# Optimization experiments

Hardware: AMD Instinct MI355X
Metric: run time of the kernel (lower is better)

## Reference

```python
import jax, jax.numpy as jnp
import numpy as np

NUM_HEADS = 32
HEAD_DIM = 128
ROPE_THETA = 10000.0


def _rope_tables(seq_len, head_dim, dtype):
    # inv freqs: 1 / theta^(2k/d), k = 0..d/2-1
    k = jnp.arange(head_dim // 2, dtype=jnp.float32)
    inv_freq = 1.0 / (ROPE_THETA ** (2.0 * k / head_dim))
    m = jnp.arange(seq_len, dtype=jnp.float32)
    freqs = jnp.outer(m, inv_freq)  # [S, D/2]
    return jnp.cos(freqs).astype(dtype), jnp.sin(freqs).astype(dtype)


def _apply_rope(x, cos, sin):
    # x: [B, H, S, D]; pairs are (x[2k], x[2k+1]) viewed as complex
    x0 = x[..., 0::2]
    x1 = x[..., 1::2]
    # broadcast cos/sin [S, D/2] -> [1, 1, S, D/2]
    out0 = x0 * cos - x1 * sin
    out1 = x0 * sin + x1 * cos
    # re-interleave
    return jnp.stack([out0, out1], axis=-1).reshape(x.shape)


def setup_inputs() -> dict:
    key = jax.random.key(0)
    k1, k2, k3 = jax.random.split(key, 3)
    B, S, D = 2, 2048, 4096
    x = jax.random.normal(k1, (B, S, D), dtype=jnp.float32)
    w_qkv = jax.random.normal(k2, (D, 3 * D), dtype=jnp.float32) * (D ** -0.5)
    w_proj = jax.random.normal(k3, (D, D), dtype=jnp.float32) * (D ** -0.5)
    b_proj = jnp.zeros((D,), dtype=jnp.float32)
    return {"x": x, "w_qkv": w_qkv, "w_proj": w_proj, "b_proj": b_proj}


def reference(x, w_qkv, w_proj, b_proj):
    B, S, D = x.shape
    H, Hd = NUM_HEADS, HEAD_DIM

    qkv = x @ w_qkv                                   # [B, S, 3D]
    qkv = qkv.reshape(B, S, 3, H, Hd)
    qkv = jnp.transpose(qkv, (2, 0, 3, 1, 4))          # [3, B, H, S, Hd]
    q, k, v = qkv[0], qkv[1], qkv[2]

    cos, sin = _rope_tables(S, Hd, x.dtype)
    q = _apply_rope(q, cos, sin)
    k = _apply_rope(k, cos, sin)

    scale = 1.0 / np.sqrt(Hd)
    scores = jnp.einsum('bhqd,bhkd->bhqk', q, k) * scale   # [B, H, S, S]
    causal = jnp.tril(jnp.ones((S, S), dtype=bool))
    scores = jnp.where(causal, scores, jnp.finfo(scores.dtype).min)
    attn = jax.nn.softmax(scores, axis=-1)
    out = jnp.einsum('bhqk,bhkd->bhqd', attn, v)            # [B, H, S, Hd]

    ctx = jnp.transpose(out, (0, 2, 1, 3)).reshape(B, S, H * Hd)
    return ctx @ w_proj + b_proj
```

## Files before the change

kernel.cpp:

```cpp
#include <hip/hip_runtime.h>
#include <stdint.h>

typedef unsigned short ushort_t;
typedef __attribute__((ext_vector_type(8))) short s16x8;
typedef __attribute__((ext_vector_type(4))) float f32x4;
typedef __attribute__((ext_vector_type(4))) unsigned short u16x4;

#define DEV __device__ __forceinline__

DEV ushort_t f2bf(float f) {
  union { float f; uint32_t u; } v; v.f = f;
  uint32_t r = (v.u + 0x7FFFu + ((v.u >> 16) & 1u)) >> 16;
  return (ushort_t)r;
}
DEV float bf2f(ushort_t u) {
  union { uint32_t u; float f; } v; v.u = ((uint32_t)u) << 16;
  return v.f;
}

DEV int swz(int row, int chunk) { return chunk ^ (row & 3) ^ ((row >> 2) & 3); }

#define GLD_LDS16(g, l)                                     \
  __builtin_amdgcn_global_load_lds(                         \
      (const __attribute__((address_space(1))) void*)(g),   \
      (__attribute__((address_space(3))) void*)(l), 16, 0, 0)

#define MFMA16(a, b, c) __builtin_amdgcn_mfma_f32_16x16x32_bf16((a), (b), (c), 0, 0, 0)

__global__ __launch_bounds__(256) void k_conv(const float* __restrict__ in,
                                              ushort_t* __restrict__ out, int n4) {
  int i = blockIdx.x * 256 + threadIdx.x;
  if (i >= n4) return;
  float4 v = ((const float4*)in)[i];
  u16x4 o;
  o[0] = f2bf(v.x); o[1] = f2bf(v.y); o[2] = f2bf(v.z); o[3] = f2bf(v.w);
  *((u16x4*)out + i) = o;
}

__global__ __launch_bounds__(256) void k_transpose_conv(const float* __restrict__ in,
                                                        ushort_t* __restrict__ out,
                                                        int R, int C) {
  __shared__ float tile[64][65];
  int c0 = blockIdx.x * 64, r0 = blockIdx.y * 64;
  int t = threadIdx.x;
#pragma unroll
  for (int i = 0; i < 4; ++i) {
    int e = (i * 256 + t) * 4;
    int rr = e >> 6, cc = e & 63;
    float4 v = *(const float4*)(in + (size_t)(r0 + rr) * C + (c0 + cc));
    tile[rr][cc] = v.x; tile[rr][cc + 1] = v.y;
    tile[rr][cc + 2] = v.z; tile[rr][cc + 3] = v.w;
  }
  __syncthreads();
#pragma unroll
  for (int i = 0; i < 4; ++i) {
    int e = (i * 256 + t) * 4;
    int cc = e >> 6, rr = e & 63;
    u16x4 o;
    o[0] = f2bf(tile[rr][cc]);     o[1] = f2bf(tile[rr + 1][cc]);
    o[2] = f2bf(tile[rr + 2][cc]); o[3] = f2bf(tile[rr + 3][cc]);
    *(u16x4*)(out + (size_t)(c0 + cc) * R + (r0 + rr)) = o;
  }
}

template <bool BF16OUT>
__global__ __launch_bounds__(256, 3) void k_gemm_bt(const ushort_t* __restrict__ A,
                                                    const ushort_t* __restrict__ Bt,
                                                    ushort_t* __restrict__ Cb,
                                                    float* __restrict__ Cf,
                                                    const float* __restrict__ bias,
                                                    int M, int N, int K) {
  __shared__ ushort_t lA[128 * 32];
  __shared__ ushort_t lB[128 * 32];
  int t = threadIdx.x;
  int wv = t >> 6, lane = t & 63, quad = lane >> 4, lrow = lane & 15;
  int wr = wv >> 1, wc = wv & 1;
  int n0 = blockIdx.x * 128, m0 = blockIdx.y * 128;

  f32x4 acc[4][4];
#pragma unroll
  for (int i = 0; i < 4; ++i)
#pragma unroll
    for (int j = 0; j < 4; ++j) acc[i][j] = (f32x4){0.f, 0.f, 0.f, 0.f};

  for (int k0 = 0; k0 < K; k0 += 32) {
    __syncthreads();
#pragma unroll
    for (int c = 0; c < 2; ++c) {
      int se = (c * 256 + t) * 8;
      int row = se >> 5;
      int scn = (se >> 3) & 3;
      int col = swz(row, scn) * 8;
      GLD_LDS16(A + (size_t)(m0 + row) * K + k0 + col, lA + (c * 256 + wv * 64) * 8);
      GLD_LDS16(Bt + (size_t)(n0 + row) * K + k0 + col, lB + (c * 256 + wv * 64) * 8);
    }
    __syncthreads();
    s16x8 af[4], bfr[4];
#pragma unroll
    for (int i = 0; i < 4; ++i) {
      int row = wr * 64 + i * 16 + lrow;
      af[i] = *(const s16x8*)(lA + row * 32 + swz(row, quad) * 8);
    }
#pragma unroll
    for (int j = 0; j < 4; ++j) {
      int row = wc * 64 + j * 16 + lrow;
      bfr[j] = *(const s16x8*)(lB + row * 32 + swz(row, quad) * 8);
    }
#pragma unroll
    for (int i = 0; i < 4; ++i)
#pragma unroll
      for (int j = 0; j < 4; ++j) acc[i][j] = MFMA16(af[i], bfr[j], acc[i][j]);
  }

#pragma unroll
  for (int i = 0; i < 4; ++i)
#pragma unroll
    for (int j = 0; j < 4; ++j)
#pragma unroll
      for (int r = 0; r < 4; ++r) {
        int gr = m0 + wr * 64 + i * 16 + quad * 4 + r;
        int gc = n0 + wc * 64 + j * 16 + lrow;
        if (BF16OUT)
          Cb[(size_t)gr * N + gc] = f2bf(acc[i][j][r]);
        else
          Cf[(size_t)gr * N + gc] = acc[i][j][r] + bias[gc];
      }
}

__global__ __launch_bounds__(256) void k_rope(ushort_t* __restrict__ qkv) {
  int tid = blockIdx.x * 256 + threadIdx.x;
  int p = tid & 63;
  int h = (tid >> 6) & 31;
  int s = (tid >> 11) & 2047;
  int b = tid >> 22;
  size_t base = (size_t)(b * 2048 + s) * 12288 + h * 128 + 2 * p;
  float inv_freq = __expf(-(float)p * 0.14391156509165667f);
  float ang = (float)s * inv_freq;
  float c = cosf(ang), sn = sinf(ang);
  float q0 = bf2f(qkv[base]), q1 = bf2f(qkv[base + 1]);
  qkv[base]        = f2bf(q0 * c - q1 * sn);
  qkv[base + 1]    = f2bf(q0 * sn + q1 * c);
  float k0 = bf2f(qkv[base + 4096]), k1 = bf2f(qkv[base + 4097]);
  qkv[base + 4096] = f2bf(k0 * c - k1 * sn);
  qkv[base + 4097] = f2bf(k0 * sn + k1 * c);
}

__global__ __launch_bounds__(256) void k_build_vt(const ushort_t* __restrict__ qkv,
                                                  ushort_t* __restrict__ vt) {
  const int S = 2048;
  int s0 = blockIdx.x * 64;
  int bh = blockIdx.y;
  int b = bh >> 5, h = bh & 31;
  __shared__ ushort_t tl[64][136];
  int t = threadIdx.x;
  const ushort_t* src = qkv + (size_t)(b * S + s0) * 12288 + 8192 + h * 128;
#pragma unroll
  for (int i = 0; i < 4; ++i) {
    int e = (i * 256 + t) * 8;
    int row = e >> 7, col = e & 127;
    *(s16x8*)&tl[row][col] = *(const s16x8*)(src + (size_t)row * 12288 + col);
  }
  __syncthreads();
  ushort_t* dst = vt + (size_t)bh * 128 * S;
#pragma unroll
  for (int i = 0; i < 4; ++i) {
    int e = (i * 256 + t) * 8;
    int d = e >> 6, ss = e & 63;
    s16x8 o;
#pragma unroll
    for (int j = 0; j < 8; ++j) o[j] = (short)tl[ss + j][d];
    *(s16x8*)(dst + (size_t)d * S + s0 + ss) = o;
  }
}

__global__ __launch_bounds__(256, 2) void k_attn(const ushort_t* __restrict__ qkv,
                                                 const ushort_t* __restrict__ vt,
                                                 ushort_t* __restrict__ ctx) {
  const int S = 2048;
  int qt = blockIdx.x, bh = blockIdx.y;
  int b = bh >> 5, h = bh & 31;
  int q0 = qt * 64;
  int t = threadIdx.x;
  int wv = t >> 6, lane = t & 63, quad = lane >> 4, lrow = lane & 15;

  __shared__ ushort_t lQ[64][136];
  __shared__ ushort_t lK[64][136];
  __shared__ ushort_t lV[128][72];
  __shared__ ushort_t lP[4][16][72];

  const ushort_t* qp = qkv + (size_t)(b * S) * 12288 + h * 128;
  const ushort_t* kp = qp + 4096;
  const ushort_t* vp = vt + (size_t)bh * 128 * S;

#pragma unroll
  for (int i = 0; i < 4; ++i) {
    int e = (i * 256 + t) * 8;
    int row = e >> 7, col = e & 127;
    *(s16x8*)&lQ[row][col] = *(const s16x8*)(qp + (size_t)(q0 + row) * 12288 + col);
  }

  f32x4 O[8];
#pragma unroll
  for (int i = 0; i < 8; ++i) O[i] = (f32x4){0.f, 0.f, 0.f, 0.f};
  float m_i[4], l_i[4];
#pragma unroll
  for (int r = 0; r < 4; ++r) { m_i[r] = -__builtin_inff(); l_i[r] = 0.f; }

  const float scale = 0.08838834764831845f;

  for (int kvt = 0; kvt <= qt; ++kvt) {
    int kv0 = kvt * 64;
    __syncthreads();
#pragma unroll
    for (int i = 0; i < 4; ++i) {
      int e = (i * 256 + t) * 8;
      int row = e >> 7, col = e & 127;
      *(s16x8*)&lK[row][col] = *(const s16x8*)(kp + (size_t)(kv0 + row) * 12288 + col);
    }
#pragma unroll
    for (int i = 0; i < 4; ++i) {
      int e = (i * 256 + t) * 8;
      int d = e >> 6, c = e & 63;
      *(s16x8*)&lV[d][c] = *(const s16x8*)(vp + (size_t)d * S + kv0 + c);
    }
    __syncthreads();

    f32x4 sc[4];
#pragma unroll
    for (int nt = 0; nt < 4; ++nt) sc[nt] = (f32x4){0.f, 0.f, 0.f, 0.f};
#pragma unroll
    for (int ks = 0; ks < 4; ++ks) {
      s16x8 a = *(const s16x8*)&lQ[wv * 16 + lrow][ks * 32 + quad * 8];
#pragma unroll
      for (int nt = 0; nt < 4; ++nt) {
        s16x8 bb = *(const s16x8*)&lK[nt * 16 + lrow][ks * 32 + quad * 8];
        sc[nt] = MFMA16(a, bb, sc[nt]);
      }
    }

    int qr = q0 + wv * 16 + quad * 4;
    float mt[4];
#pragma unroll
    for (int r = 0; r < 4; ++r) mt[r] = -__builtin_inff();
    float pvl[4][4];
#pragma unroll
    for (int nt = 0; nt < 4; ++nt) {
      int kc = kv0 + nt * 16 + lrow;
#pragma unroll
      for (int r = 0; r < 4; ++r) {
        float sv = sc[nt][r] * scale;
        if (kc > qr + r) sv = -__builtin_inff();
        pvl[nt][r] = sv;
        mt[r] = fmaxf(mt[r], sv);
      }
    }
#pragma unroll
    for (int r = 0; r < 4; ++r)
#pragma unroll
      for (int off = 1; off < 16; off <<= 1)
        mt[r] = fmaxf(mt[r], __shfl_xor(mt[r], off, 16));

    float al[4], ls[4];
#pragma unroll
    for (int r = 0; r < 4; ++r) {
      float mn = fmaxf(m_i[r], mt[r]);
      al[r] = __expf(m_i[r] - mn);
      m_i[r] = mn;
      ls[r] = 0.f;
    }
#pragma unroll
    for (int nt = 0; nt < 4; ++nt)
#pragma unroll
      for (int r = 0; r < 4; ++r) {
        float p = __expf(pvl[nt][r] - m_i[r]);
        ushort_t pu = f2bf(p);
        lP[wv][quad * 4 + r][nt * 16 + lrow] = pu;
        ls[r] += bf2f(pu);
      }
#pragma unroll
    for (int r = 0; r < 4; ++r) {
#pragma unroll
      for (int off = 1; off < 16; off <<= 1) ls[r] += __shfl_xor(ls[r], off, 16);
      l_i[r] = al[r] * l_i[r] + ls[r];
    }
#pragma unroll
    for (int f = 0; f < 8; ++f)
#pragma unroll
      for (int r = 0; r < 4; ++r) O[f][r] *= al[r];
    __syncthreads();

#pragma unroll
    for (int ks = 0; ks < 2; ++ks) {
      s16x8 a = *(const s16x8*)&lP[wv][lrow][ks * 32 + quad * 8];
#pragma unroll
      for (int f = 0; f < 8; ++f) {
        s16x8 bb = *(const s16x8*)&lV[f * 16 + lrow][ks * 32 + quad * 8];
        O[f] = MFMA16(a, bb, O[f]);
      }
    }
  }

#pragma unroll
  for (int r = 0; r < 4; ++r) l_i[r] = 1.f / l_i[r];
#pragma unroll
  for (int f = 0; f < 8; ++f)
#pragma unroll
    for (int r = 0; r < 4; ++r) {
      size_t idx = (size_t)(b * S + q0 + wv * 16 + quad * 4 + r) * 4096 + h * 128 + f * 16 + lrow;
      ctx[idx] = f2bf(O[f][r] * l_i[r]);
    }
}

extern "C" void kernel_launch(void* const* d_in, const int* in_sizes, int n_in,
                              void* d_out, int out_size, void* d_ws, size_t ws_size,
                              hipStream_t stream) {
  const float* x      = (const float*)d_in[0];
  const float* w_qkv  = (const float*)d_in[1];
  const float* w_proj = (const float*)d_in[2];
  const float* b_proj = (const float*)d_in[3];
  float* out = (float*)d_out;

  char* ws = (char*)d_ws;
  ushort_t* xb     = (ushort_t*)(ws);
  ushort_t* wqkvt  = (ushort_t*)(ws + 33554432ULL);
  ushort_t* wprojt = (ushort_t*)(ws + 134217728ULL);
  ushort_t* qkvb   = (ushort_t*)(ws + 167772160ULL);
  ushort_t* vt     = (ushort_t*)(ws + 268435456ULL);
  ushort_t* ctx    = (ushort_t*)(ws + 301989888ULL);

  k_conv<<<16384, 256, 0, stream>>>(x, xb, 16777216 / 4);
  k_transpose_conv<<<dim3(192, 64), 256, 0, stream>>>(w_qkv, wqkvt, 4096, 12288);
  k_transpose_conv<<<dim3(64, 64), 256, 0, stream>>>(w_proj, wprojt, 4096, 4096);
  k_gemm_bt<true><<<dim3(96, 32), 256, 0, stream>>>(xb, wqkvt, qkvb, nullptr, nullptr,
                                                    4096, 12288, 4096);
  k_rope<<<32768, 256, 0, stream>>>(qkvb);
  k_build_vt<<<dim3(32, 64), 256, 0, stream>>>(qkvb, vt);
  k_attn<<<dim3(32, 64), 256, 0, stream>>>(qkvb, vt, ctx);
  k_gemm_bt<false><<<dim3(32, 32), 256, 0, stream>>>(ctx, wprojt, nullptr, out, b_proj,
                                                     4096, 4096, 4096);
}
```

Before: 1.424 ms.

## Fuse RoPE into QKV GEMM epilogue and widen attention query tile

Applies RoPE inside the QKV GEMM epilogue, pairing adjacent columns with a lane shuffle, and removes the separate rope kernel together with its read-modify-write pass over Q and K. The attention kernel now handles 128 query rows per block, keeps Q fragments in registers instead of LDS, and loads K and V tiles with direct global-to-LDS loads into XOR-swizzled layouts. This halves the number of K/V tile loads per query and cuts LDS bank conflicts. In exchange it costs more registers (two sets of O accumulators), adds a sincos per output element in the GEMM epilogue, and causal imbalance grows with the coarser query tiles.

```diff
diff --git a/kernel.cpp b/kernel.cpp
--- a/kernel.cpp
+++ b/kernel.cpp
@@ -63,7 +63,7 @@
   }
 }
 
-template <bool BF16OUT>
+template <bool BF16OUT, bool ROPE>
 __global__ __launch_bounds__(256, 3) void k_gemm_bt(const ushort_t* __restrict__ A,
                                                     const ushort_t* __restrict__ Bt,
                                                     ushort_t* __restrict__ Cb,
@@ -112,37 +112,34 @@
       for (int j = 0; j < 4; ++j) acc[i][j] = MFMA16(af[i], bfr[j], acc[i][j]);
   }
 
-#pragma unroll
-  for (int i = 0; i < 4; ++i)
-#pragma unroll
-    for (int j = 0; j < 4; ++j)
+  bool do_rope = ROPE && (n0 < 8192);
+  float sgn_sel = (lrow & 1) ? 1.f : -1.f;
+#pragma unroll
+  for (int j = 0; j < 4; ++j) {
+    int gc = n0 + wc * 64 + j * 16 + lrow;
+    float freq = 0.f;
+    if (do_rope) {
+      int p = (gc & 127) >> 1;
+      freq = __expf(-(float)p * 0.14391156509165667f);
+    }
+#pragma unroll
+    for (int i = 0; i < 4; ++i)
 #pragma unroll
       for (int r = 0; r < 4; ++r) {
         int gr = m0 + wr * 64 + i * 16 + quad * 4 + r;
-        int gc = n0 + wc * 64 + j * 16 + lrow;
+        float val = acc[i][j][r];
+        if (do_rope) {
+          float other = __shfl_xor(val, 1);
+          float sv, cv;
+          sincosf((float)(gr & 2047) * freq, &sv, &cv);
+          val = fmaf(other, sgn_sel * sv, val * cv);
+        }
         if (BF16OUT)
-          Cb[(size_t)gr * N + gc] = f2bf(acc[i][j][r]);
+          Cb[(size_t)gr * N + gc] = f2bf(val);
         else
-          Cf[(size_t)gr * N + gc] = acc[i][j][r] + bias[gc];
-      }
-}
-
-__global__ __launch_bounds__(256) void k_rope(ushort_t* __restrict__ qkv) {
-  int tid = blockIdx.x * 256 + threadIdx.x;
-  int p = tid & 63;
-  int h = (tid >> 6) & 31;
-  int s = (tid >> 11) & 2047;
-  int b = tid >> 22;
-  size_t base = (size_t)(b * 2048 + s) * 12288 + h * 128 + 2 * p;
-  float inv_freq = __expf(-(float)p * 0.14391156509165667f);
-  float ang = (float)s * inv_freq;
-  float c = cosf(ang), sn = sinf(ang);
-  float q0 = bf2f(qkv[base]), q1 = bf2f(qkv[base + 1]);
-  qkv[base]        = f2bf(q0 * c - q1 * sn);
-  qkv[base + 1]    = f2bf(q0 * sn + q1 * c);
-  float k0 = bf2f(qkv[base + 4096]), k1 = bf2f(qkv[base + 4097]);
-  qkv[base + 4096] = f2bf(k0 * c - k1 * sn);
-  qkv[base + 4097] = f2bf(k0 * sn + k1 * c);
+          Cf[(size_t)gr * N + gc] = val + bias[gc];
+      }
+  }
 }
 
 __global__ __launch_bounds__(256) void k_build_vt(const ushort_t* __restrict__ qkv,
@@ -179,136 +176,165 @@
   const int S = 2048;
   int qt = blockIdx.x, bh = blockIdx.y;
   int b = bh >> 5, h = bh & 31;
-  int q0 = qt * 64;
+  int q0 = qt * 128;
   int t = threadIdx.x;
   int wv = t >> 6, lane = t & 63, quad = lane >> 4, lrow = lane & 15;
 
-  __shared__ ushort_t lQ[64][136];
-  __shared__ ushort_t lK[64][136];
-  __shared__ ushort_t lV[128][72];
-  __shared__ ushort_t lP[4][16][72];
+  __shared__ ushort_t lK[64 * 128];
+  __shared__ ushort_t lV[128 * 64];
+  __shared__ ushort_t lP[4][32][72];
 
   const ushort_t* qp = qkv + (size_t)(b * S) * 12288 + h * 128;
   const ushort_t* kp = qp + 4096;
   const ushort_t* vp = vt + (size_t)bh * 128 * S;
 
-#pragma unroll
-  for (int i = 0; i < 4; ++i) {
-    int e = (i * 256 + t) * 8;
-    int row = e >> 7, col = e & 127;
-    *(s16x8*)&lQ[row][col] = *(const s16x8*)(qp + (size_t)(q0 + row) * 12288 + col);
-  }
-
-  f32x4 O[8];
-#pragma unroll
-  for (int i = 0; i < 8; ++i) O[i] = (f32x4){0.f, 0.f, 0.f, 0.f};
-  float m_i[4], l_i[4];
-#pragma unroll
-  for (int r = 0; r < 4; ++r) { m_i[r] = -__builtin_inff(); l_i[r] = 0.f; }
+  s16x8 qf[2][4];
+  int qrb = q0 + wv * 32;
+#pragma unroll
+  for (int ti = 0; ti < 2; ++ti)
+#pragma unroll
+    for (int ks = 0; ks < 4; ++ks)
+      qf[ti][ks] = *(const s16x8*)(qp + (size_t)(qrb + ti * 16 + lrow) * 12288 +
+                                   ks * 32 + quad * 8);
+
+  f32x4 O[2][8];
+#pragma unroll
+  for (int ti = 0; ti < 2; ++ti)
+#pragma unroll
+    for (int f = 0; f < 8; ++f) O[ti][f] = (f32x4){0.f, 0.f, 0.f, 0.f};
+  float m_i[2][4], l_i[2][4];
+#pragma unroll
+  for (int ti = 0; ti < 2; ++ti)
+#pragma unroll
+    for (int r = 0; r < 4; ++r) { m_i[ti][r] = -__builtin_inff(); l_i[ti][r] = 0.f; }
 
   const float scale = 0.08838834764831845f;
-
-  for (int kvt = 0; kvt <= qt; ++kvt) {
-    int kv0 = kvt * 64;
+  int qhi = q0 + 127;
+
+  for (int kv0 = 0; kv0 <= qhi; kv0 += 64) {
     __syncthreads();
-#pragma unroll
-    for (int i = 0; i < 4; ++i) {
-      int e = (i * 256 + t) * 8;
-      int row = e >> 7, col = e & 127;
-      *(s16x8*)&lK[row][col] = *(const s16x8*)(kp + (size_t)(kv0 + row) * 12288 + col);
-    }
-#pragma unroll
-    for (int i = 0; i < 4; ++i) {
-      int e = (i * 256 + t) * 8;
-      int d = e >> 6, c = e & 63;
-      *(s16x8*)&lV[d][c] = *(const s16x8*)(vp + (size_t)d * S + kv0 + c);
+    {
+      int ck = lane & 15;
+      int cv = lane & 7;
+#pragma unroll
+      for (int it = 0; it < 4; ++it) {
+        int slot = wv * 4 + it;
+        int rowk = slot * 4 + (lane >> 4);
+        int cpk = (ck & 8) | ((ck & 7) ^ (rowk & 7));
+        GLD_LDS16(kp + (size_t)(kv0 + rowk) * 12288 + cpk * 8, lK + slot * 512);
+        int rowv = slot * 8 + (lane >> 3);
+        int cpv = cv ^ (rowv & 7);
+        GLD_LDS16(vp + (size_t)rowv * S + kv0 + cpv * 8, lV + slot * 512);
+      }
     }
     __syncthreads();
 
-    f32x4 sc[4];
-#pragma unroll
-    for (int nt = 0; nt < 4; ++nt) sc[nt] = (f32x4){0.f, 0.f, 0.f, 0.f};
+    f32x4 sc[2][4];
+#pragma unroll
+    for (int ti = 0; ti < 2; ++ti)
+#pragma unroll
+      for (int nt = 0; nt < 4; ++nt) sc[ti][nt] = (f32x4){0.f, 0.f, 0.f, 0.f};
 #pragma unroll
     for (int ks = 0; ks < 4; ++ks) {
-      s16x8 a = *(const s16x8*)&lQ[wv * 16 + lrow][ks * 32 + quad * 8];
+      s16x8 bk[4];
 #pragma unroll
       for (int nt = 0; nt < 4; ++nt) {
-        s16x8 bb = *(const s16x8*)&lK[nt * 16 + lrow][ks * 32 + quad * 8];
-        sc[nt] = MFMA16(a, bb, sc[nt]);
-      }
-    }
-
-    int qr = q0 + wv * 16 + quad * 4;
-    float mt[4];
-#pragma unroll
-    for (int r = 0; r < 4; ++r) mt[r] = -__builtin_inff();
-    float pvl[4][4];
-#pragma unroll
-    for (int nt = 0; nt < 4; ++nt) {
-      int kc = kv0 + nt * 16 + lrow;
+        int row = nt * 16 + lrow;
+        int cc = ks * 4 + quad;
+        int cp = (cc & 8) | ((cc & 7) ^ (row & 7));
+        bk[nt] = *(const s16x8*)(lK + row * 128 + cp * 8);
+      }
+#pragma unroll
+      for (int ti = 0; ti < 2; ++ti)
+#pragma unroll
+        for (int nt = 0; nt < 4; ++nt) sc[ti][nt] = MFMA16(qf[ti][ks], bk[nt], sc[ti][nt]);
+    }
+
+#pragma unroll
+    for (int ti = 0; ti < 2; ++ti) {
+      int qr = qrb + ti * 16 + quad * 4;
+      float mt[4];
+#pragma unroll
+      for (int r = 0; r < 4; ++r) mt[r] = -__builtin_inff();
+      float pvl[4][4];
+#pragma unroll
+      for (int nt = 0; nt < 4; ++nt) {
+        int kc = kv0 + nt * 16 + lrow;
+#pragma unroll
+        for (int r = 0; r < 4; ++r) {
+          float sv = sc[ti][nt][r] * scale;
+          if (kc > qr + r) sv = -__builtin_inff();
+          pvl[nt][r] = sv;
+          mt[r] = fmaxf(mt[r], sv);
+        }
+      }
+#pragma unroll
+      for (int r = 0; r < 4; ++r)
+#pragma unroll
+        for (int off = 1; off < 16; off <<= 1)
+          mt[r] = fmaxf(mt[r], __shfl_xor(mt[r], off, 16));
+
+      float al[4], ls[4];
 #pragma unroll
       for (int r = 0; r < 4; ++r) {
-        float sv = sc[nt][r] * scale;
-        if (kc > qr + r) sv = -__builtin_inff();
-        pvl[nt][r] = sv;
-        mt[r] = fmaxf(mt[r], sv);
-      }
-    }
-#pragma unroll
-    for (int r = 0; r < 4; ++r)
-#pragma unroll
-      for (int off = 1; off < 16; off <<= 1)
-        mt[r] = fmaxf(mt[r], __shfl_xor(mt[r], off, 16));
-
-    float al[4], ls[4];
-#pragma unroll
-    for (int r = 0; r < 4; ++r) {
-      float mn = fmaxf(m_i[r], mt[r]);
-      al[r] = __expf(m_i[r] - mn);
-      m_i[r] = mn;
-      ls[r] = 0.f;
-    }
-#pragma unroll
-    for (int nt = 0; nt < 4; ++nt)
+        float mn = fmaxf(m_i[ti][r], mt[r]);
+        al[r] = __expf(m_i[ti][r] - mn);
+        m_i[ti][r] = mn;
+        ls[r] = 0.f;
+      }
+#pragma unroll
+      for (int nt = 0; nt < 4; ++nt)
+#pragma unroll
+        for (int r = 0; r < 4; ++r) {
+          float p = __expf(pvl[nt][r] - m_i[ti][r]);
+          ushort_t pu = f2bf(p);
+          lP[wv][ti * 16 + quad * 4 + r][nt * 16 + lrow] = pu;
+          ls[r] += bf2f(pu);
+        }
 #pragma unroll
       for (int r = 0; r < 4; ++r) {
-        float p = __expf(pvl[nt][r] - m_i[r]);
-        ushort_t pu = f2bf(p);
-        lP[wv][quad * 4 + r][nt * 16 + lrow] = pu;
-        ls[r] += bf2f(pu);
-      }
-#pragma unroll
-    for (int r = 0; r < 4; ++r) {
-#pragma unroll
-      for (int off = 1; off < 16; off <<= 1) ls[r] += __shfl_xor(ls[r], off, 16);
-      l_i[r] = al[r] * l_i[r] + ls[r];
-    }
+#pragma unroll
+        for (int off = 1; off < 16; off <<= 1) ls[r] += __shfl_xor(ls[r], off, 16);
+        l_i[ti][r] = al[r] * l_i[ti][r] + ls[r];
+      }
+#pragma unroll
+      for (int f = 0; f < 8; ++f)
+#pragma unroll
+        for (int r = 0; r < 4; ++r) O[ti][f][r] *= al[r];
+    }
+
+#pragma unroll
+    for (int ks = 0; ks < 2; ++ks) {
+      s16x8 pa[2];
+#pragma unroll
+      for (int ti = 0; ti < 2; ++ti)
+        pa[ti] = *(const s16x8*)&lP[wv][ti * 16 + lrow][ks * 32 + quad * 8];
+#pragma unroll
+      for (int f = 0; f < 8; ++f) {
+        int row = f * 16 + lrow;
+        int cc = ks * 4 + quad;
+        int cp = cc ^ (row & 7);
+        s16x8 bv = *(const s16x8*)(lV + row * 64 + cp * 8);
+#pragma unroll
+        for (int ti = 0; ti < 2; ++ti) O[ti][f] = MFMA16(pa[ti], bv, O[ti][f]);
+      }
+    }
+  }
+
+#pragma unroll
+  for (int ti = 0; ti < 2; ++ti) {
+    float inv[4];
+#pragma unroll
+    for (int r = 0; r < 4; ++r) inv[r] = 1.f / l_i[ti][r];
 #pragma unroll
     for (int f = 0; f < 8; ++f)
 #pragma unroll
-      for (int r = 0; r < 4; ++r) O[f][r] *= al[r];
-    __syncthreads();
-
-#pragma unroll
-    for (int ks = 0; ks < 2; ++ks) {
-      s16x8 a = *(const s16x8*)&lP[wv][lrow][ks * 32 + quad * 8];
-#pragma unroll
-      for (int f = 0; f < 8; ++f) {
-        s16x8 bb = *(const s16x8*)&lV[f * 16 + lrow][ks * 32 + quad * 8];
-        O[f] = MFMA16(a, bb, O[f]);
-      }
-    }
-  }
-
-#pragma unroll
-  for (int r = 0; r < 4; ++r) l_i[r] = 1.f / l_i[r];
-#pragma unroll
-  for (int f = 0; f < 8; ++f)
-#pragma unroll
-    for (int r = 0; r < 4; ++r) {
-      size_t idx = (size_t)(b * S + q0 + wv * 16 + quad * 4 + r) * 4096 + h * 128 + f * 16 + lrow;
-      ctx[idx] = f2bf(O[f][r] * l_i[r]);
-    }
+      for (int r = 0; r < 4; ++r) {
+        size_t idx = (size_t)(b * S + qrb + ti * 16 + quad * 4 + r) * 4096 +
+                     h * 128 + f * 16 + lrow;
+        ctx[idx] = f2bf(O[ti][f][r] * inv[r]);
+      }
+  }
 }
 
 extern "C" void kernel_launch(void* const* d_in, const int* in_sizes, int n_in,
@@ -331,11 +357,10 @@
   k_conv<<<16384, 256, 0, stream>>>(x, xb, 16777216 / 4);
   k_transpose_conv<<<dim3(192, 64), 256, 0, stream>>>(w_qkv, wqkvt, 4096, 12288);
   k_transpose_conv<<<dim3(64, 64), 256, 0, stream>>>(w_proj, wprojt, 4096, 4096);
-  k_gemm_bt<true><<<dim3(96, 32), 256, 0, stream>>>(xb, wqkvt, qkvb, nullptr, nullptr,
-                                                    4096, 12288, 4096);
-  k_rope<<<32768, 256, 0, stream>>>(qkvb);
+  k_gemm_bt<true, true><<<dim3(96, 32), 256, 0, stream>>>(xb, wqkvt, qkvb, nullptr,
+                                                          nullptr, 4096, 12288, 4096);
   k_build_vt<<<dim3(32, 64), 256, 0, stream>>>(qkvb, vt);
-  k_attn<<<dim3(32, 64), 256, 0, stream>>>(qkvb, vt, ctx);
-  k_gemm_bt<false><<<dim3(32, 32), 256, 0, stream>>>(ctx, wprojt, nullptr, out, b_proj,
-                                                     4096, 4096, 4096);
-}
+  k_attn<<<dim3(16, 64), 256, 0, stream>>>(qkvb, vt, ctx);
+  k_gemm_bt<false, false><<<dim3(32, 32), 256, 0, stream>>>(ctx, wprojt, nullptr, out,
+                                                            b_proj, 4096, 4096, 4096);
+}
```

Result: faster. 1.383 ms (-2.9%).
